# Optimization experiments

Hardware: AMD Instinct MI355X
Metric: run time of the kernel (lower is better)

## Reference

```python
import jax, jax.numpy as jnp
import numpy as np

N_NODES = 50000
N_EDGES = 625000
IN_CH = 128
OUT_CH = 128


def setup_inputs() -> dict:
    key = jax.random.key(0)
    k1, k2, k3, k4 = jax.random.split(key, 4)
    x = jax.random.normal(k1, (N_NODES, IN_CH), dtype=jnp.float32)
    edge_index = jax.random.randint(k2, (2, N_EDGES), 0, N_NODES, dtype=jnp.int64)
    # nn.Linear(in, out): weight [out, in], bias [out]
    bound = 1.0 / np.sqrt(IN_CH)
    W = jax.random.uniform(k3, (OUT_CH, IN_CH), minval=-bound, maxval=bound, dtype=jnp.float32)
    b = jax.random.uniform(k4, (OUT_CH,), minval=-bound, maxval=bound, dtype=jnp.float32)
    return {"x": x, "edge_index": edge_index, "W": W, "b": b}


def reference(x, edge_index, W, b):
    row, col = edge_index[0], edge_index[1]
    num_nodes = x.shape[0]
    # degree of destination nodes (scatter_add of ones over row)
    deg = jax.ops.segment_sum(jnp.ones(row.shape[0], dtype=x.dtype), row,
                              num_segments=num_nodes)
    deg_inv_sqrt = jnp.where(deg > 0, jax.lax.rsqrt(jnp.maximum(deg, 1.0)) * jnp.where(deg > 0, 1.0, 0.0), 0.0)
    deg_inv_sqrt = jnp.where(deg > 0, deg ** -0.5, 0.0)
    norm = deg_inv_sqrt[row] * deg_inv_sqrt[col]  # [E]
    src = x[col] * norm[:, None]                  # gather + scale, [E, C]
    out = jax.ops.segment_sum(src, row, num_segments=num_nodes)  # scatter-add
    return out @ W.T + b
```

## Files before the change

kernel.cpp:

```cpp
#include <hip/hip_runtime.h>
#include <hip/hip_bf16.h>

#define NN 50000
#define NE 625000
#define CH 128
#define RSTR 32

typedef __attribute__((ext_vector_type(8))) short short8;
typedef __attribute__((ext_vector_type(4))) float floatx4;

__device__ __forceinline__ ushort f2bf(float v) {
    __hip_bfloat16 h = __float2bfloat16(v);
    return *(ushort*)&h;
}
__device__ __forceinline__ float bf2f(uint u) {
    return __uint_as_float(u << 16);
}
__device__ __forceinline__ float inv_sqrt_deg(int d) {
    return (d > 0) ? rsqrtf((float)d) : 0.0f;
}

__global__ __launch_bounds__(256) void k_prep(const float* __restrict__ x,
                                              ushort* __restrict__ xb,
                                              const float* __restrict__ W,
                                              ushort* __restrict__ whi,
                                              ushort* __restrict__ wlo,
                                              const int* __restrict__ row,
                                              const int* __restrict__ col,
                                              uint* __restrict__ csr) {
    int b = blockIdx.x;
    if (b < 2442) {
        int t = b * 256 + threadIdx.x;
        if (t < NE) {
            int r = row[t];
            int c = col[t];
            int p = (int)atomicAdd(&csr[r * RSTR], 1u);
            if (p < 62)
                ((ushort*)(csr + r * RSTR))[2 + p] = (ushort)c;
        }
    } else if (b < 8692) {
        int i = ((b - 2442) * 256 + threadIdx.x) * 4;
        float4 v = *(const float4*)(x + i);
        ushort4 o;
        o.x = f2bf(v.x); o.y = f2bf(v.y); o.z = f2bf(v.z); o.w = f2bf(v.w);
        *(ushort4*)(xb + i) = o;
    } else {
        int i = (b - 8692) * 256 + threadIdx.x;
        float v = W[i];
        ushort h = f2bf(v);
        whi[i] = h;
        wlo[i] = f2bf(v - bf2f((uint)h));
    }
}

__global__ __launch_bounds__(256) void k_nrm(const uint* __restrict__ csr,
                                             int* __restrict__ deg_c,
                                             float* __restrict__ nrm) {
    int i = blockIdx.x * 256 + threadIdx.x;
    if (i < NN) {
        int d = (int)csr[i * RSTR];
        deg_c[i] = d;
        nrm[i] = inv_sqrt_deg(d);
    } else if (i < 50176) {
        deg_c[i] = 0;
        nrm[i] = 0.0f;
    }
}

__global__ __launch_bounds__(256) void k_agg(const ushort* __restrict__ xb,
                                             const int* __restrict__ deg_c,
                                             const float* __restrict__ nrm,
                                             const uint* __restrict__ csr,
                                             ushort* __restrict__ ahi) {
    const int wave = threadIdx.x >> 6;
    const int lane = threadIdx.x & 63;
    const int node = blockIdx.x * 4 + wave;
    const int deg = deg_c[node];
    const float dr = nrm[node];

    const ushort* slots = (const ushort*)(csr + node * RSTR) + 2;
    int li = (lane < 62) ? lane : 0;
    ushort craw = slots[li];
    int cli = (lane < deg) ? (int)craw : 0;
    float nl = (lane < deg) ? nrm[cli] : 0.0f;

    float ax = 0.0f, ay = 0.0f;
    for (int j = 0; j < deg; j += 8) {
#pragma unroll
        for (int u = 0; u < 8; ++u) {
            int cc = __shfl(cli, j + u);
            float nn = __shfl(nl, j + u);
            ushort2 v = ((const ushort2*)(xb + (size_t)cc * CH))[lane];
            ax = fmaf(bf2f((uint)v.x), nn, ax);
            ay = fmaf(bf2f((uint)v.y), nn, ay);
        }
    }

    ushort2 hv;
    hv.x = f2bf(ax * dr);
    hv.y = f2bf(ay * dr);
    ((ushort2*)(ahi + (size_t)node * CH))[lane] = hv;
}

__global__ __launch_bounds__(256) void k_mfma(const ushort* __restrict__ ahi,
                                              const ushort* __restrict__ whi,
                                              const ushort* __restrict__ wlo,
                                              const float* __restrict__ bias,
                                              float* __restrict__ out) {
    const int wave = threadIdx.x >> 6;
    const int lane = threadIdx.x & 63;
    const int quad = lane >> 4;
    const int r16 = lane & 15;
    const int m0 = blockIdx.x * 32;
    const int nt0 = wave * 2, nt1 = nt0 + 1;

    const ushort* a0p  = ahi + (size_t)(m0 + r16) * CH + quad * 8;
    const ushort* a1p  = a0p + 16 * CH;
    const ushort* bh0p = whi + (size_t)(nt0 * 16 + r16) * CH + quad * 8;
    const ushort* bl0p = wlo + (size_t)(nt0 * 16 + r16) * CH + quad * 8;
    const ushort* bh1p = whi + (size_t)(nt1 * 16 + r16) * CH + quad * 8;
    const ushort* bl1p = wlo + (size_t)(nt1 * 16 + r16) * CH + quad * 8;

    float b0 = bias[nt0 * 16 + r16];
    float b1 = bias[nt1 * 16 + r16];
    floatx4 acc00 = {b0, b0, b0, b0};
    floatx4 acc01 = {b1, b1, b1, b1};
    floatx4 acc10 = {b0, b0, b0, b0};
    floatx4 acc11 = {b1, b1, b1, b1};

#pragma unroll
    for (int kb = 0; kb < 4; ++kb) {
        const int k0 = kb * 32;
        short8 a0 = *(const short8*)(a0p + k0);
        short8 a1 = *(const short8*)(a1p + k0);
        short8 h0 = *(const short8*)(bh0p + k0);
        short8 l0 = *(const short8*)(bl0p + k0);
        short8 h1 = *(const short8*)(bh1p + k0);
        short8 l1 = *(const short8*)(bl1p + k0);
        acc00 = __builtin_amdgcn_mfma_f32_16x16x32_bf16(a0, h0, acc00, 0, 0, 0);
        acc00 = __builtin_amdgcn_mfma_f32_16x16x32_bf16(a0, l0, acc00, 0, 0, 0);
        acc01 = __builtin_amdgcn_mfma_f32_16x16x32_bf16(a0, h1, acc01, 0, 0, 0);
        acc01 = __builtin_amdgcn_mfma_f32_16x16x32_bf16(a0, l1, acc01, 0, 0, 0);
        acc10 = __builtin_amdgcn_mfma_f32_16x16x32_bf16(a1, h0, acc10, 0, 0, 0);
        acc10 = __builtin_amdgcn_mfma_f32_16x16x32_bf16(a1, l0, acc10, 0, 0, 0);
        acc11 = __builtin_amdgcn_mfma_f32_16x16x32_bf16(a1, h1, acc11, 0, 0, 0);
        acc11 = __builtin_amdgcn_mfma_f32_16x16x32_bf16(a1, l1, acc11, 0, 0, 0);
    }

#pragma unroll
    for (int r = 0; r < 4; ++r) {
        int row0 = m0 + quad * 4 + r;
        int row1 = row0 + 16;
        if (row0 < NN) {
            out[(size_t)row0 * CH + nt0 * 16 + r16] = acc00[r];
            out[(size_t)row0 * CH + nt1 * 16 + r16] = acc01[r];
        }
        if (row1 < NN) {
            out[(size_t)row1 * CH + nt0 * 16 + r16] = acc10[r];
            out[(size_t)row1 * CH + nt1 * 16 + r16] = acc11[r];
        }
    }
}

extern "C" void kernel_launch(void* const* d_in, const int* in_sizes, int n_in,
                              void* d_out, int out_size, void* d_ws, size_t ws_size,
                              hipStream_t stream) {
    const float* x = (const float*)d_in[0];
    const int* ei = (const int*)d_in[1];
    const float* W = (const float*)d_in[2];
    const float* b = (const float*)d_in[3];
    float* out = (float*)d_out;

    uint* csr = (uint*)d_ws;
    int* deg_c = (int*)(csr + (size_t)NN * RSTR);
    float* nrm = (float*)(deg_c + 50176);
    ushort* ahi = (ushort*)(nrm + 50176);
    ushort* xb = ahi + (size_t)(NN + 16) * CH;
    ushort* whi = xb + (size_t)NN * CH;
    ushort* wlo = whi + CH * CH;

    hipMemsetAsync(csr, 0, (size_t)NN * RSTR * sizeof(uint), stream);
    k_prep<<<8756, 256, 0, stream>>>(x, xb, W, whi, wlo, ei, ei + NE, csr);
    k_nrm<<<196, 256, 0, stream>>>(csr, deg_c, nrm);
    k_agg<<<NN / 4, 256, 0, stream>>>(xb, deg_c, nrm, csr, ahi);
    k_mfma<<<(NN + 31) / 32, 256, 0, stream>>>(ahi, whi, wlo, b, out);
}
```

Measured before the change: 162.1 us.

## Build CSR via two-pass LDS bucket sort instead of global atomics

Edges are first binned by destination group (256 rows) using per-block LDS histograms, prefix sums and one global atomic per group, then written packed into per-group segments. A second kernel builds each row's neighbor slots in LDS and writes the full CSR rows, degrees and norms, removing the large CSR memset and the scattered global atomics. This trades those costs for an extra pass over the edges and four reads of each group segment, plus a fixed per-group capacity that could drop edges on skewed inputs.

```diff
diff --git a/kernel.cpp b/kernel.cpp
--- a/kernel.cpp
+++ b/kernel.cpp
@@ -5,6 +5,10 @@
 #define NE 625000
 #define CH 128
 #define RSTR 32
+#define NG 196
+#define GCAP 4096
+#define NBIN 256
+#define EPB 2442
 
 typedef __attribute__((ext_vector_type(8))) short short8;
 typedef __attribute__((ext_vector_type(4))) float floatx4;
@@ -15,9 +19,6 @@
 }
 __device__ __forceinline__ float bf2f(uint u) {
     return __uint_as_float(u << 16);
-}
-__device__ __forceinline__ float inv_sqrt_deg(int d) {
-    return (d > 0) ? rsqrtf((float)d) : 0.0f;
 }
 
 __global__ __launch_bounds__(256) void k_prep(const float* __restrict__ x,
@@ -27,43 +28,134 @@
                                               ushort* __restrict__ wlo,
                                               const int* __restrict__ row,
                                               const int* __restrict__ col,
-                                              uint* __restrict__ csr) {
+                                              uint* __restrict__ gbase,
+                                              uint* __restrict__ gseg) {
+    __shared__ uint h[NG];
+    __shared__ uint sc[NG];
+    __shared__ uint gb[NG];
+    __shared__ uint cur[NG];
+    __shared__ uint ss[256];
+    __shared__ uint pk[EPB];
+
     int b = blockIdx.x;
-    if (b < 2442) {
-        int t = b * 256 + threadIdx.x;
-        if (t < NE) {
-            int r = row[t];
-            int c = col[t];
-            int p = (int)atomicAdd(&csr[r * RSTR], 1u);
-            if (p < 62)
-                ((ushort*)(csr + r * RSTR))[2 + p] = (ushort)c;
-        }
-    } else if (b < 8692) {
-        int i = ((b - 2442) * 256 + threadIdx.x) * 4;
+    int t = threadIdx.x;
+    if (b < NBIN) {
+        int e0 = b * EPB;
+        int n = NE - e0; if (n > EPB) n = EPB;
+
+        for (int i = t; i < NG; i += 256) h[i] = 0;
+        __syncthreads();
+
+        int r[10], c[10];
+#pragma unroll
+        for (int j = 0; j < 10; ++j) {
+            int i = t + j * 256;
+            int idx = (i < n) ? (e0 + i) : e0;
+            r[j] = row[idx];
+            c[j] = col[idx];
+        }
+#pragma unroll
+        for (int j = 0; j < 10; ++j)
+            if (t + j * 256 < n) atomicAdd(&h[r[j] >> 8], 1u);
+        __syncthreads();
+
+        ss[t] = (t < NG) ? h[t] : 0u;
+        __syncthreads();
+        for (int off = 1; off < 256; off <<= 1) {
+            uint add = (t >= off) ? ss[t - off] : 0u;
+            __syncthreads();
+            ss[t] += add;
+            __syncthreads();
+        }
+        if (t < NG) {
+            uint ex = (t == 0) ? 0u : ss[t - 1];
+            sc[t] = ex;
+            cur[t] = ex;
+            if (h[t] > 0) gb[t] = atomicAdd(&gbase[t], h[t]);
+        }
+        __syncthreads();
+
+#pragma unroll
+        for (int j = 0; j < 10; ++j) {
+            if (t + j * 256 < n) {
+                int g = r[j] >> 8;
+                uint p = atomicAdd(&cur[g], 1u);
+                pk[p] = ((uint)(r[j] & 255) << 16) | (uint)(c[j] & 0xffff);
+            }
+        }
+        __syncthreads();
+
+        for (int i = t; i < n; i += 256) {
+            int lo = 0, hi = NG - 1;
+            while (lo < hi) {
+                int mid = (lo + hi + 1) >> 1;
+                if (sc[mid] <= (uint)i) lo = mid; else hi = mid - 1;
+            }
+            int g = lo;
+            uint off = gb[g] + ((uint)i - sc[g]);
+            if (off < GCAP) gseg[(size_t)g * GCAP + off] = pk[i];
+        }
+    } else if (b < 6506) {
+        int i = ((b - 256) * 256 + t) * 4;
         float4 v = *(const float4*)(x + i);
         ushort4 o;
         o.x = f2bf(v.x); o.y = f2bf(v.y); o.z = f2bf(v.z); o.w = f2bf(v.w);
         *(ushort4*)(xb + i) = o;
     } else {
-        int i = (b - 8692) * 256 + threadIdx.x;
+        int i = (b - 6506) * 256 + t;
         float v = W[i];
-        ushort h = f2bf(v);
-        whi[i] = h;
-        wlo[i] = f2bf(v - bf2f((uint)h));
-    }
-}
-
-__global__ __launch_bounds__(256) void k_nrm(const uint* __restrict__ csr,
+        ushort hh = f2bf(v);
+        whi[i] = hh;
+        wlo[i] = f2bf(v - bf2f((uint)hh));
+    }
+}
+
+__global__ __launch_bounds__(256) void k_csr(const uint* __restrict__ gseg,
+                                             const uint* __restrict__ gcnt,
+                                             uint* __restrict__ csr,
                                              int* __restrict__ deg_c,
                                              float* __restrict__ nrm) {
-    int i = blockIdx.x * 256 + threadIdx.x;
-    if (i < NN) {
-        int d = (int)csr[i * RSTR];
-        deg_c[i] = d;
-        nrm[i] = inv_sqrt_deg(d);
-    } else if (i < 50176) {
-        deg_c[i] = 0;
-        nrm[i] = 0.0f;
+    __shared__ ushort slots[64][62];
+    __shared__ uint dcnt[64];
+    int g = blockIdx.x >> 2;
+    int q = blockIdx.x & 3;
+    int t = threadIdx.x;
+
+    int n = (int)gcnt[g];
+    if (n > GCAP) n = GCAP;
+    if (t < 64) dcnt[t] = 0;
+    __syncthreads();
+
+    const uint* seg = gseg + (size_t)g * GCAP;
+    for (int i = t; i < n; i += 256) {
+        uint p = seg[i];
+        int rl = (int)(p >> 16);
+        if ((rl >> 6) == q) {
+            int r6 = rl & 63;
+            uint k = atomicAdd(&dcnt[r6], 1u);
+            if (k < 62) slots[r6][k] = (ushort)(p & 0xffff);
+        }
+    }
+    __syncthreads();
+
+    int row0 = g * 256 + q * 64;
+    for (int i = t; i < 2048; i += 256) {
+        int rl = i >> 5, w = i & 31;
+        int rr = row0 + rl;
+        if (rr < NN) {
+            uint val;
+            if (w == 0) val = dcnt[rl];
+            else val = (uint)slots[rl][2 * w - 2] | ((uint)slots[rl][2 * w - 1] << 16);
+            csr[(size_t)rr * RSTR + w] = val;
+        }
+    }
+    if (t < 64) {
+        int rr = row0 + t;
+        if (rr < NN) {
+            int d = (int)dcnt[t];
+            deg_c[rr] = d;
+            nrm[rr] = (d > 0) ? rsqrtf((float)d) : 0.0f;
+        }
     }
 }
 
@@ -178,10 +270,12 @@
     ushort* xb = ahi + (size_t)(NN + 16) * CH;
     ushort* whi = xb + (size_t)NN * CH;
     ushort* wlo = whi + CH * CH;
-
-    hipMemsetAsync(csr, 0, (size_t)NN * RSTR * sizeof(uint), stream);
-    k_prep<<<8756, 256, 0, stream>>>(x, xb, W, whi, wlo, ei, ei + NE, csr);
-    k_nrm<<<196, 256, 0, stream>>>(csr, deg_c, nrm);
+    uint* gbase = (uint*)(wlo + CH * CH);
+    uint* gseg = gbase + 256;
+
+    hipMemsetAsync(gbase, 0, NG * sizeof(uint), stream);
+    k_prep<<<6570, 256, 0, stream>>>(x, xb, W, whi, wlo, ei, ei + NE, gbase, gseg);
+    k_csr<<<NG * 4, 256, 0, stream>>>(gseg, gbase, csr, deg_c, nrm);
     k_agg<<<NN / 4, 256, 0, stream>>>(xb, deg_c, nrm, csr, ahi);
     k_mfma<<<(NN + 31) / 32, 256, 0, stream>>>(ahi, whi, wlo, b, out);
 }
```

After: 145.5 us. -10.2%, faster.
